# Kernel tuning notes

Hardware: AMD Instinct MI355X
Metric: run time of the kernel (lower is better)

The kernel has to match this reference:

```python
import jax, jax.numpy as jnp
import numpy as np
import math

SIGMA = 1.0
TRUNC = 4.0
N_STEPS = 6
SIZE = 160  # D = H = W


def make_gaussian_kernel(sigma=SIGMA, truncated=TRUNC):
    # erf-integrated Gaussian, matching gaussian_1d(approx='erf', normalize=True)
    tail = int(max(sigma * truncated, 0.5) + 0.5)
    x = np.arange(-tail, tail + 1, dtype=np.float64)
    t = 0.70710678 / abs(sigma)
    out = np.array([0.5 * (math.erf(t * (xi + 0.5)) - math.erf(t * (xi - 0.5))) for xi in x])
    out = np.clip(out, 0.0, None)
    out = out / out.sum()
    return jnp.asarray(out, dtype=jnp.float32)


def identity_grid(D, H, W):
    # torch grid_sample convention: last dim is (x, y, z) ~ (W, H, D), align_corners=True
    zs = jnp.linspace(-1.0, 1.0, D, dtype=jnp.float32)
    ys = jnp.linspace(-1.0, 1.0, H, dtype=jnp.float32)
    xs = jnp.linspace(-1.0, 1.0, W, dtype=jnp.float32)
    zz, yy, xx = jnp.meshgrid(zs, ys, xs, indexing='ij')  # [D,H,W]
    return jnp.stack([xx, yy, zz], axis=-1)[None]  # [1,D,H,W,3]


def separable_gaussian_3d(x, kernel):
    # x: [B,C,D,H,W]; grouped 1D conv along each spatial axis, zero padding
    C = x.shape[1]
    k = kernel.shape[0]
    pad = (k - 1) // 2
    for d in range(3):
        kshape = [1, 1, 1]
        kshape[d] = k
        w = jnp.broadcast_to(kernel.reshape(1, 1, *kshape), (C, 1, *kshape))
        padding = [(0, 0), (0, 0), (0, 0)]
        padding[d] = (pad, pad)
        x = jax.lax.conv_general_dilated(
            x, w, window_strides=(1, 1, 1), padding=padding,
            dimension_numbers=('NCDHW', 'OIDHW', 'NCDHW'), feature_group_count=C)
    return x


def grid_sample_3d(img, grid):
    # img: [B,C,D,H,W]; grid: [B,D,H,W,3] (x,y,z in [-1,1]); trilinear,
    # align_corners=True, padding_mode='zeros' (torch defaults)
    B, C, D, H, W = img.shape
    x = (grid[..., 0] + 1.0) * 0.5 * (W - 1)
    y = (grid[..., 1] + 1.0) * 0.5 * (H - 1)
    z = (grid[..., 2] + 1.0) * 0.5 * (D - 1)
    x0 = jnp.floor(x); y0 = jnp.floor(y); z0 = jnp.floor(z)
    wx1 = x - x0; wy1 = y - y0; wz1 = z - z0
    wx = (1.0 - wx1, wx1); wy = (1.0 - wy1, wy1); wz = (1.0 - wz1, wz1)

    def gather(zi, yi, xi):
        # zi,yi,xi: [B,D,H,W] float corner indices
        valid = ((zi >= 0) & (zi <= D - 1) & (yi >= 0) & (yi <= H - 1)
                 & (xi >= 0) & (xi <= W - 1)).astype(img.dtype)
        zc = jnp.clip(zi, 0, D - 1).astype(jnp.int32)
        yc = jnp.clip(yi, 0, H - 1).astype(jnp.int32)
        xc = jnp.clip(xi, 0, W - 1).astype(jnp.int32)

        def one(imgc, zc1, yc1, xc1, v1):
            return imgc[:, zc1, yc1, xc1] * v1[None]  # [C,D,H,W]
        return jax.vmap(one)(img, zc, yc, xc, valid)

    out = jnp.zeros_like(img)
    for iz in (0, 1):
        for iy in (0, 1):
            for ix in (0, 1):
                w = (wz[iz] * wy[iy] * wx[ix])[:, None]  # [B,1,D,H,W]
                out = out + gather(z0 + iz, y0 + iy, x0 + ix) * w
    return out


def setup_inputs() -> dict:
    key = jax.random.key(0)
    k1, _ = jax.random.split(key)
    D = H = W = SIZE
    velocity = 0.1 * jax.random.normal(k1, (1, D, H, W, 3), dtype=jnp.float32)
    grid = identity_grid(D, H, W)
    gauss_kernel = make_gaussian_kernel()
    return {"velocity": velocity, "grid": grid, "gauss_kernel": gauss_kernel, "n_steps": N_STEPS}


def reference(velocity, grid, gauss_kernel, n_steps):
    # 1) Gaussian-smooth the momentum/velocity field (separable_filtering)
    vimg = jnp.transpose(velocity, (0, 4, 1, 2, 3))  # [B,3,D,H,W]
    vimg = separable_gaussian_3d(vimg, gauss_kernel)
    v = jnp.transpose(vimg, (0, 2, 3, 4, 1))  # [B,D,H,W,3]
    # 2) scaling and squaring: v <- v + v o (grid + v), n times
    v = v * (1.0 / (2 ** n_steps))
    for _ in range(n_steps):
        vi = jnp.transpose(v, (0, 4, 1, 2, 3))
        v = v + jnp.transpose(grid_sample_3d(vi, v + grid), (0, 2, 3, 4, 1))
    return v
```

## Files before the change

### kernel.cpp

```cpp
#include <hip/hip_runtime.h>


constexpr int W = 160, H = 160, D = 160;
constexpr int NVOX = W * H * D;
constexpr int NSTEPS = 6;
constexpr float HSC = 79.5f;
constexpr int SEG = 16;
constexpr int WIN = SEG + 8;

__device__ __forceinline__ int iclamp(int v, int lo, int hi) {
    return v < lo ? lo : (v > hi ? hi : v);
}

__global__ void blur_z_win(const float* __restrict__ in, float* __restrict__ out,
                           const float* __restrict__ gk)
{
    int tid = blockIdx.x * blockDim.x + threadIdx.x;
    int x = tid % W;
    int r = tid / W;
    int y = r % H;
    int seg = r / H;
    int z0 = seg * SEG;

    const size_t PS = (size_t)W * H * 3;
    size_t colBase = ((size_t)y * W + x) * 3;

    float kw[9];
#pragma unroll
    for (int t = 0; t < 9; ++t) kw[t] = gk[t];

    float win[WIN][3];
    if (z0 >= 4 && z0 + SEG + 4 <= D) {
        const float* p0 = in + (size_t)(z0 - 4) * PS + colBase;
#pragma unroll
        for (int j = 0; j < WIN; ++j) {
            const float* p = p0 + (size_t)j * PS;
            win[j][0] = p[0]; win[j][1] = p[1]; win[j][2] = p[2];
        }
    } else {
#pragma unroll
        for (int j = 0; j < WIN; ++j) {
            int zz = z0 - 4 + j;
            bool ok = (zz >= 0) && (zz < D);
            const float* p = in + (size_t)iclamp(zz, 0, D - 1) * PS + colBase;
            win[j][0] = ok ? p[0] : 0.f;
            win[j][1] = ok ? p[1] : 0.f;
            win[j][2] = ok ? p[2] : 0.f;
        }
    }

#pragma unroll
    for (int t = 0; t < SEG; ++t) {
        float a0 = 0.f, a1 = 0.f, a2 = 0.f;
#pragma unroll
        for (int k = 0; k < 9; ++k) {
            a0 = fmaf(kw[k], win[t + k][0], a0);
            a1 = fmaf(kw[k], win[t + k][1], a1);
            a2 = fmaf(kw[k], win[t + k][2], a2);
        }
        float* q = out + (size_t)(z0 + t) * PS + colBase;
        q[0] = a0; q[1] = a1; q[2] = a2;
    }
}

__global__ void blur_y_win(const float* __restrict__ in, float* __restrict__ out,
                           const float* __restrict__ gk)
{
    int tid = blockIdx.x * blockDim.x + threadIdx.x;
    int x = tid % W;
    int r = tid / W;
    int z = r % D;
    int seg = r / D;
    int y0 = seg * SEG;

    const size_t RS = (size_t)W * 3;
    size_t base = ((size_t)z * H * W + x) * 3;

    float kw[9];
#pragma unroll
    for (int t = 0; t < 9; ++t) kw[t] = gk[t];

    float win[WIN][3];
    if (y0 >= 4 && y0 + SEG + 4 <= H) {
        const float* p0 = in + base + (size_t)(y0 - 4) * RS;
#pragma unroll
        for (int j = 0; j < WIN; ++j) {
            const float* p = p0 + (size_t)j * RS;
            win[j][0] = p[0]; win[j][1] = p[1]; win[j][2] = p[2];
        }
    } else {
#pragma unroll
        for (int j = 0; j < WIN; ++j) {
            int yy = y0 - 4 + j;
            bool ok = (yy >= 0) && (yy < H);
            const float* p = in + base + (size_t)iclamp(yy, 0, H - 1) * RS;
            win[j][0] = ok ? p[0] : 0.f;
            win[j][1] = ok ? p[1] : 0.f;
            win[j][2] = ok ? p[2] : 0.f;
        }
    }

#pragma unroll
    for (int t = 0; t < SEG; ++t) {
        float a0 = 0.f, a1 = 0.f, a2 = 0.f;
#pragma unroll
        for (int k = 0; k < 9; ++k) {
            a0 = fmaf(kw[k], win[t + k][0], a0);
            a1 = fmaf(kw[k], win[t + k][1], a1);
            a2 = fmaf(kw[k], win[t + k][2], a2);
        }
        float* q = out + base + (size_t)(y0 + t) * RS;
        q[0] = a0; q[1] = a1; q[2] = a2;
    }
}

__global__ void blur_x_vec4(const float* __restrict__ in, float* __restrict__ out,
                            const float* __restrict__ gk, float scale)
{
    int tid = blockIdx.x * blockDim.x + threadIdx.x;
    if (tid >= NVOX / 4) return;
    int nx4 = W / 4;
    int x0 = (tid % nx4) * 4;
    int row = tid / nx4;
    size_t rowBase = (size_t)row * W * 3;

    float kw[9];
#pragma unroll
    for (int t = 0; t < 9; ++t) kw[t] = gk[t];

    long f0 = (long)rowBase + (long)(x0 - 4) * 3;
    const long maxF4 = (long)NVOX * 3 - 4;
    float wv[36];
#pragma unroll
    for (int k = 0; k < 9; ++k) {
        long a = f0 + 4 * k;
        a = a < 0 ? 0 : (a > maxF4 ? maxF4 : a);
        float4 v4 = *(const float4*)(in + a);
        wv[4 * k + 0] = v4.x; wv[4 * k + 1] = v4.y;
        wv[4 * k + 2] = v4.z; wv[4 * k + 3] = v4.w;
    }
#pragma unroll
    for (int m = 0; m < 12; ++m) {
        int xi = x0 - 4 + m;
        if (xi < 0 || xi >= W) { wv[3 * m] = 0.f; wv[3 * m + 1] = 0.f; wv[3 * m + 2] = 0.f; }
    }

    float o[12];
#pragma unroll
    for (int j = 0; j < 4; ++j) {
#pragma unroll
        for (int c = 0; c < 3; ++c) {
            float s = 0.f;
#pragma unroll
            for (int t = 0; t < 9; ++t) s = fmaf(kw[t], wv[3 * (j + t) + c], s);
            o[3 * j + c] = s * scale;
        }
    }
    float4* q = (float4*)(out + rowBase + (size_t)x0 * 3);
    q[0] = make_float4(o[0], o[1], o[2],  o[3]);
    q[1] = make_float4(o[4], o[5], o[6],  o[7]);
    q[2] = make_float4(o[8], o[9], o[10], o[11]);
}

__global__ void step_kernel(const float* __restrict__ v, float* __restrict__ out)
{
    int b = blockIdx.x;
    int bs = (b & 7) * 2000 + (b >> 3);
    int i = bs * blockDim.x + threadIdx.x;
    int x = i % W;
    int t = i / W;
    int y = t % H;
    int z = t / H;

    const float* pv = v + (size_t)i * 3;
    float vx = pv[0], vy = pv[1], vz = pv[2];

    float sx = fmaf(vx, HSC, (float)x);
    float sy = fmaf(vy, HSC, (float)y);
    float sz = fmaf(vz, HSC, (float)z);

    float fx = floorf(sx), fy = floorf(sy), fz = floorf(sz);
    int x0 = (int)fx, y0 = (int)fy, z0 = (int)fz;
    float wx1 = sx - fx, wy1 = sy - fy, wz1 = sz - fz;
    float wx0 = 1.f - wx1, wy0 = 1.f - wy1, wz0 = 1.f - wz1;

    wx0 *= (x0     >= 0 && x0     < W) ? 1.f : 0.f;
    wx1 *= (x0 + 1 >= 0 && x0 + 1 < W) ? 1.f : 0.f;
    wy0 *= (y0     >= 0 && y0     < H) ? 1.f : 0.f;
    wy1 *= (y0 + 1 >= 0 && y0 + 1 < H) ? 1.f : 0.f;
    wz0 *= (z0     >= 0 && z0     < D) ? 1.f : 0.f;
    wz1 *= (z0 + 1 >= 0 && z0 + 1 < D) ? 1.f : 0.f;

    int xc0 = iclamp(x0, 0, W - 1), xc1 = iclamp(x0 + 1, 0, W - 1);
    int yc0 = iclamp(y0, 0, H - 1), yc1 = iclamp(y0 + 1, 0, H - 1);
    int zc0 = iclamp(z0, 0, D - 1), zc1 = iclamp(z0 + 1, 0, D - 1);

    int idx[8];
    idx[0] = (zc0 * H + yc0) * W + xc0;
    idx[1] = (zc0 * H + yc0) * W + xc1;
    idx[2] = (zc0 * H + yc1) * W + xc0;
    idx[3] = (zc0 * H + yc1) * W + xc1;
    idx[4] = (zc1 * H + yc0) * W + xc0;
    idx[5] = (zc1 * H + yc0) * W + xc1;
    idx[6] = (zc1 * H + yc1) * W + xc0;
    idx[7] = (zc1 * H + yc1) * W + xc1;

    float c[8][3];
#pragma unroll
    for (int k = 0; k < 8; ++k) {
        const float* p = v + (size_t)idx[k] * 3;
        c[k][0] = p[0];
        c[k][1] = p[1];
        c[k][2] = p[2];
    }

    float w8[8];
    w8[0] = wz0 * wy0 * wx0;
    w8[1] = wz0 * wy0 * wx1;
    w8[2] = wz0 * wy1 * wx0;
    w8[3] = wz0 * wy1 * wx1;
    w8[4] = wz1 * wy0 * wx0;
    w8[5] = wz1 * wy0 * wx1;
    w8[6] = wz1 * wy1 * wx0;
    w8[7] = wz1 * wy1 * wx1;

    float r0 = vx, r1 = vy, r2 = vz;
#pragma unroll
    for (int k = 0; k < 8; ++k) {
        r0 = fmaf(w8[k], c[k][0], r0);
        r1 = fmaf(w8[k], c[k][1], r1);
        r2 = fmaf(w8[k], c[k][2], r2);
    }

    float* q = out + (size_t)i * 3;
    q[0] = r0;
    q[1] = r1;
    q[2] = r2;
}

extern "C" void kernel_launch(void* const* d_in, const int* in_sizes, int n_in,
                              void* d_out, int out_size, void* d_ws, size_t ws_size,
                              hipStream_t stream)
{
    const float* vel = (const float*)d_in[0];
    const float* gk  = (const float*)d_in[2];

    float* OUT = (float*)d_out;
    float* WS  = (float*)d_ws;

    const int threads = 256;
    const int winBlocks = (W * H * (D / SEG)) / threads;
    const int x4Blocks  = (NVOX / 4) / threads;
    const int stepBlocks = NVOX / threads;
    const float scale = 1.0f / (float)(1 << NSTEPS);

    blur_z_win <<<winBlocks, threads, 0, stream>>>(vel, OUT, gk);
    blur_y_win <<<winBlocks, threads, 0, stream>>>(OUT, WS, gk);
    blur_x_vec4<<<x4Blocks, threads, 0, stream>>>(WS, OUT, gk, scale);

    step_kernel<<<stepBlocks, threads, 0, stream>>>(OUT, WS);
    step_kernel<<<stepBlocks, threads, 0, stream>>>(WS, OUT);
    step_kernel<<<stepBlocks, threads, 0, stream>>>(OUT, WS);
    step_kernel<<<stepBlocks, threads, 0, stream>>>(WS, OUT);
    step_kernel<<<stepBlocks, threads, 0, stream>>>(OUT, WS);
    step_kernel<<<stepBlocks, threads, 0, stream>>>(WS, OUT);
}
```

Baseline: 242.2 us.

## Fuse Y and X blur passes into one shared-memory tiled kernel

Replaces the separate Y-blur and X-blur kernels with a single kernel that loads a 24x88 halo tile of one z-plane into LDS, applies the Y filter into a second LDS buffer, then applies the X filter and scale before writing out. This removes one full read and write of the 3-channel volume and one kernel launch. The Z-blur segment length is halved to 8 to expose more parallelism, and both blur kernels get an XCD-style block index swizzle. The added halo loads, two barriers and LDS traffic are the cost, and the smaller Z segment raises redundant halo reads.

```diff
diff --git a/kernel.cpp b/kernel.cpp
--- a/kernel.cpp
+++ b/kernel.cpp
@@ -5,8 +5,14 @@
 constexpr int NVOX = W * H * D;
 constexpr int NSTEPS = 6;
 constexpr float HSC = 79.5f;
-constexpr int SEG = 16;
-constexpr int WIN = SEG + 8;
+
+constexpr int ZSEG = 8;
+constexpr int ZWIN = ZSEG + 8;
+
+constexpr int YT = 16;
+constexpr int XT = 80;
+constexpr int YR = YT + 8;
+constexpr int XR = XT + 8;
 
 __device__ __forceinline__ int iclamp(int v, int lo, int hi) {
     return v < lo ? lo : (v > hi ? hi : v);
@@ -15,12 +21,14 @@
 __global__ void blur_z_win(const float* __restrict__ in, float* __restrict__ out,
                            const float* __restrict__ gk)
 {
-    int tid = blockIdx.x * blockDim.x + threadIdx.x;
+    int b = blockIdx.x;
+    int bs = (b & 7) * 250 + (b >> 3);
+    int tid = bs * blockDim.x + threadIdx.x;
     int x = tid % W;
     int r = tid / W;
     int y = r % H;
     int seg = r / H;
-    int z0 = seg * SEG;
+    int z0 = seg * ZSEG;
 
     const size_t PS = (size_t)W * H * 3;
     size_t colBase = ((size_t)y * W + x) * 3;
@@ -29,17 +37,17 @@
 #pragma unroll
     for (int t = 0; t < 9; ++t) kw[t] = gk[t];
 
-    float win[WIN][3];
-    if (z0 >= 4 && z0 + SEG + 4 <= D) {
+    float win[ZWIN][3];
+    if (z0 >= 4 && z0 + ZSEG + 4 <= D) {
         const float* p0 = in + (size_t)(z0 - 4) * PS + colBase;
 #pragma unroll
-        for (int j = 0; j < WIN; ++j) {
+        for (int j = 0; j < ZWIN; ++j) {
             const float* p = p0 + (size_t)j * PS;
             win[j][0] = p[0]; win[j][1] = p[1]; win[j][2] = p[2];
         }
     } else {
 #pragma unroll
-        for (int j = 0; j < WIN; ++j) {
+        for (int j = 0; j < ZWIN; ++j) {
             int zz = z0 - 4 + j;
             bool ok = (zz >= 0) && (zz < D);
             const float* p = in + (size_t)iclamp(zz, 0, D - 1) * PS + colBase;
@@ -50,7 +58,7 @@
     }
 
 #pragma unroll
-    for (int t = 0; t < SEG; ++t) {
+    for (int t = 0; t < ZSEG; ++t) {
         float a0 = 0.f, a1 = 0.f, a2 = 0.f;
 #pragma unroll
         for (int k = 0; k < 9; ++k) {
@@ -63,103 +71,72 @@
     }
 }
 
-__global__ void blur_y_win(const float* __restrict__ in, float* __restrict__ out,
-                           const float* __restrict__ gk)
-{
-    int tid = blockIdx.x * blockDim.x + threadIdx.x;
-    int x = tid % W;
-    int r = tid / W;
-    int z = r % D;
-    int seg = r / D;
-    int y0 = seg * SEG;
-
-    const size_t RS = (size_t)W * 3;
-    size_t base = ((size_t)z * H * W + x) * 3;
+__global__ void blur_yx_fused(const float* __restrict__ in, float* __restrict__ out,
+                              const float* __restrict__ gk, float scale)
+{
+    __shared__ float raw[YR][XR][3];
+    __shared__ float yb [YT][XR][3];
+
+    int b = blockIdx.x;
+    int bs = (b & 7) * 400 + (b >> 3);
+    int xh   = bs % 2;
+    int t2   = bs / 2;
+    int yseg = t2 % 10;
+    int z    = t2 / 10;
+    int y0 = yseg * YT;
+    int x0 = xh * XT;
 
     float kw[9];
 #pragma unroll
     for (int t = 0; t < 9; ++t) kw[t] = gk[t];
 
-    float win[WIN][3];
-    if (y0 >= 4 && y0 + SEG + 4 <= H) {
-        const float* p0 = in + base + (size_t)(y0 - 4) * RS;
-#pragma unroll
-        for (int j = 0; j < WIN; ++j) {
-            const float* p = p0 + (size_t)j * RS;
-            win[j][0] = p[0]; win[j][1] = p[1]; win[j][2] = p[2];
-        }
-    } else {
-#pragma unroll
-        for (int j = 0; j < WIN; ++j) {
-            int yy = y0 - 4 + j;
-            bool ok = (yy >= 0) && (yy < H);
-            const float* p = in + base + (size_t)iclamp(yy, 0, H - 1) * RS;
-            win[j][0] = ok ? p[0] : 0.f;
-            win[j][1] = ok ? p[1] : 0.f;
-            win[j][2] = ok ? p[2] : 0.f;
-        }
-    }
-
-#pragma unroll
-    for (int t = 0; t < SEG; ++t) {
+    const size_t planeBase = (size_t)z * H * W * 3;
+
+    for (int j = threadIdx.x; j < YR * XR; j += 256) {
+        int col = j % XR;
+        int row = j / XR;
+        int yy = y0 - 4 + row;
+        int xx = x0 - 4 + col;
+        bool ok = (yy >= 0) && (yy < H) && (xx >= 0) && (xx < W);
+        const float* p = in + planeBase +
+            ((size_t)iclamp(yy, 0, H - 1) * W + iclamp(xx, 0, W - 1)) * 3;
+        raw[row][col][0] = ok ? p[0] : 0.f;
+        raw[row][col][1] = ok ? p[1] : 0.f;
+        raw[row][col][2] = ok ? p[2] : 0.f;
+    }
+    __syncthreads();
+
+    for (int j = threadIdx.x; j < YT * XR; j += 256) {
+        int col = j % XR;
+        int row = j / XR;
         float a0 = 0.f, a1 = 0.f, a2 = 0.f;
 #pragma unroll
         for (int k = 0; k < 9; ++k) {
-            a0 = fmaf(kw[k], win[t + k][0], a0);
-            a1 = fmaf(kw[k], win[t + k][1], a1);
-            a2 = fmaf(kw[k], win[t + k][2], a2);
-        }
-        float* q = out + base + (size_t)(y0 + t) * RS;
-        q[0] = a0; q[1] = a1; q[2] = a2;
-    }
-}
-
-__global__ void blur_x_vec4(const float* __restrict__ in, float* __restrict__ out,
-                            const float* __restrict__ gk, float scale)
-{
-    int tid = blockIdx.x * blockDim.x + threadIdx.x;
-    if (tid >= NVOX / 4) return;
-    int nx4 = W / 4;
-    int x0 = (tid % nx4) * 4;
-    int row = tid / nx4;
-    size_t rowBase = (size_t)row * W * 3;
-
-    float kw[9];
-#pragma unroll
-    for (int t = 0; t < 9; ++t) kw[t] = gk[t];
-
-    long f0 = (long)rowBase + (long)(x0 - 4) * 3;
-    const long maxF4 = (long)NVOX * 3 - 4;
-    float wv[36];
-#pragma unroll
-    for (int k = 0; k < 9; ++k) {
-        long a = f0 + 4 * k;
-        a = a < 0 ? 0 : (a > maxF4 ? maxF4 : a);
-        float4 v4 = *(const float4*)(in + a);
-        wv[4 * k + 0] = v4.x; wv[4 * k + 1] = v4.y;
-        wv[4 * k + 2] = v4.z; wv[4 * k + 3] = v4.w;
-    }
-#pragma unroll
-    for (int m = 0; m < 12; ++m) {
-        int xi = x0 - 4 + m;
-        if (xi < 0 || xi >= W) { wv[3 * m] = 0.f; wv[3 * m + 1] = 0.f; wv[3 * m + 2] = 0.f; }
-    }
-
-    float o[12];
-#pragma unroll
-    for (int j = 0; j < 4; ++j) {
-#pragma unroll
-        for (int c = 0; c < 3; ++c) {
-            float s = 0.f;
-#pragma unroll
-            for (int t = 0; t < 9; ++t) s = fmaf(kw[t], wv[3 * (j + t) + c], s);
-            o[3 * j + c] = s * scale;
-        }
-    }
-    float4* q = (float4*)(out + rowBase + (size_t)x0 * 3);
-    q[0] = make_float4(o[0], o[1], o[2],  o[3]);
-    q[1] = make_float4(o[4], o[5], o[6],  o[7]);
-    q[2] = make_float4(o[8], o[9], o[10], o[11]);
+            a0 = fmaf(kw[k], raw[row + k][col][0], a0);
+            a1 = fmaf(kw[k], raw[row + k][col][1], a1);
+            a2 = fmaf(kw[k], raw[row + k][col][2], a2);
+        }
+        yb[row][col][0] = a0;
+        yb[row][col][1] = a1;
+        yb[row][col][2] = a2;
+    }
+    __syncthreads();
+
+    for (int j = threadIdx.x; j < YT * XT; j += 256) {
+        int xo = j % XT;
+        int yo = j / XT;
+        float a0 = 0.f, a1 = 0.f, a2 = 0.f;
+#pragma unroll
+        for (int k = 0; k < 9; ++k) {
+            a0 = fmaf(kw[k], yb[yo][xo + k][0], a0);
+            a1 = fmaf(kw[k], yb[yo][xo + k][1], a1);
+            a2 = fmaf(kw[k], yb[yo][xo + k][2], a2);
+        }
+        float* q = out + planeBase + ((size_t)(y0 + yo) * W + (x0 + xo)) * 3;
+        q[0] = a0 * scale;
+        q[1] = a1 * scale;
+        q[2] = a2 * scale;
+    }
 }
 
 __global__ void step_kernel(const float* __restrict__ v, float* __restrict__ out)
@@ -249,14 +226,13 @@
     float* WS  = (float*)d_ws;
 
     const int threads = 256;
-    const int winBlocks = (W * H * (D / SEG)) / threads;
-    const int x4Blocks  = (NVOX / 4) / threads;
+    const int zBlocks   = (W * H * (D / ZSEG)) / threads;
+    const int yxBlocks  = D * (H / YT) * (W / XT);
     const int stepBlocks = NVOX / threads;
     const float scale = 1.0f / (float)(1 << NSTEPS);
 
-    blur_z_win <<<winBlocks, threads, 0, stream>>>(vel, OUT, gk);
-    blur_y_win <<<winBlocks, threads, 0, stream>>>(OUT, WS, gk);
-    blur_x_vec4<<<x4Blocks, threads, 0, stream>>>(WS, OUT, gk, scale);
+    blur_z_win   <<<zBlocks,  threads, 0, stream>>>(vel, WS, gk);
+    blur_yx_fused<<<yxBlocks, threads, 0, stream>>>(WS, OUT, gk, scale);
 
     step_kernel<<<stepBlocks, threads, 0, stream>>>(OUT, WS);
     step_kernel<<<stepBlocks, threads, 0, stream>>>(WS, OUT);
```

Result: no change. 239.5 us (-1.1%).
